# Kernel tuning notes

Measured on AMD Instinct MI355X. Metric: run time of the kernel, lower is better.

## Reference

```python
import jax, jax.numpy as jnp
import numpy as np

N_NODES = 100000
N_EDGES = 3200000
N_GRAPHS = 256
NEG_SLOPE = 0.2  # PyG GATConv default


def setup_inputs() -> dict:
    key = jax.random.key(0)
    ks = jax.random.split(key, 20)
    x = jax.random.normal(ks[0], (N_NODES, 20), jnp.float32)
    edge_index = jax.random.randint(ks[1], (2, N_EDGES), 0, N_NODES, dtype=jnp.int32)
    batch = jnp.sort(jax.random.randint(ks[2], (N_NODES,), 0, N_GRAPHS, dtype=jnp.int32))
    s = 0.1
    return {
        "x": x,
        "edge_index": edge_index,
        "batch": batch,
        "num_graphs": N_GRAPHS,
        "w_gat": jax.random.normal(ks[3], (20, 4, 16), jnp.float32) * s,
        "att_src": jax.random.normal(ks[4], (4, 16), jnp.float32) * s,
        "att_dst": jax.random.normal(ks[5], (4, 16), jnp.float32) * s,
        "b_gat": jax.random.normal(ks[6], (64,), jnp.float32) * s,
        "w_fuse": jax.random.normal(ks[7], (64, 64), jnp.float32) * s,
        "b_fuse": jax.random.normal(ks[8], (64,), jnp.float32) * s,
        "w_h1": jax.random.normal(ks[9], (64, 32), jnp.float32) * s,
        "b_h1": jax.random.normal(ks[10], (32,), jnp.float32) * s,
        "w_h2": jax.random.normal(ks[11], (32, 16), jnp.float32) * s,
        "b_h2": jax.random.normal(ks[12], (16,), jnp.float32) * s,
        "w_h3": jax.random.normal(ks[13], (16, 16), jnp.float32) * s,
        "b_h3": jax.random.normal(ks[14], (16,), jnp.float32) * s,
        "w_ev": jax.random.normal(ks[15], (16, 3), jnp.float32) * s,
        "b_ev": jax.random.normal(ks[16], (3,), jnp.float32) * s,
        "w_env": jax.random.normal(ks[17], (16, 3), jnp.float32) * s,
        "b_env": jax.random.normal(ks[18], (3,), jnp.float32) * s,
    }


def gat_conv(x, edge_index, w_gat, att_src, att_dst, b_gat, num_nodes):
    # Linear projection per head: [N, H, C]
    xh = jnp.einsum('nf,fhc->nhc', x, w_gat)
    # add self loops (PyG add_self_loops=True)
    loop = jnp.arange(num_nodes, dtype=edge_index.dtype)
    src = jnp.concatenate([edge_index[0], loop])  # source j
    dst = jnp.concatenate([edge_index[1], loop])  # target i
    # per-node attention terms [N, H]
    a_s = jnp.einsum('nhc,hc->nh', xh, att_src)
    a_d = jnp.einsum('nhc,hc->nh', xh, att_dst)
    # per-edge logit, leaky relu
    logit = jax.nn.leaky_relu(a_s[src] + a_d[dst], NEG_SLOPE)  # [E, H]
    # segment softmax over destination node
    m = jax.ops.segment_max(logit, dst, num_segments=num_nodes)
    e = jnp.exp(logit - m[dst])
    z = jax.ops.segment_sum(e, dst, num_segments=num_nodes)
    alpha = e / z[dst]  # [E, H]
    # weighted scatter-aggregate of source features
    msg = xh[src] * alpha[:, :, None]  # [E, H, C]
    out = jax.ops.segment_sum(msg, dst, num_segments=num_nodes)  # [N, H, C]
    return out.reshape(num_nodes, -1) + b_gat  # concat heads + bias


def reference(x, edge_index, batch, num_graphs, w_gat, att_src, att_dst, b_gat,
              w_fuse, b_fuse, w_h1, b_h1, w_h2, b_h2, w_h3, b_h3,
              w_ev, b_ev, w_env, b_env):
    n = x.shape[0]
    h = gat_conv(x, edge_index, w_gat, att_src, att_dst, b_gat, n)
    h = jax.nn.relu(h @ w_fuse + b_fuse)
    h = jax.nn.relu(h @ w_h1 + b_h1)
    h = jax.nn.relu(h @ w_h2 + b_h2)
    h = jax.nn.relu(h @ w_h3 + b_h3)
    # global mean pool over graphs
    sums = jax.ops.segment_sum(h, batch, num_segments=num_graphs)
    cnts = jax.ops.segment_sum(jnp.ones((n, 1), h.dtype), batch, num_segments=num_graphs)
    g = sums / jnp.maximum(cnts, 1.0)
    out_event = g @ w_ev + b_ev
    out_env = g @ w_env + b_env
    return (out_event, out_env)
```

## Files before the change

kernel.cpp:

```cpp
#include <hip/hip_runtime.h>
#include <hip/hip_bf16.h>
#include <hip/hip_fp16.h>

#define FIN 20
#define HEADS 4
#define F 64
#define NEG_SLOPE 0.2f
#define AP 68
#define BSHIFT 8
#define BMASK 255
#define BCAP 9216
#define MAXBUCK 512
#define BIN_EPT 16

__global__ void __launch_bounds__(256)
prep_bin(const float* __restrict__ x,
         const float* __restrict__ w_gat,
         const float* __restrict__ att_src,
         const float* __restrict__ att_dst,
         __half* __restrict__ xh,
         float* __restrict__ a_s,
         float* __restrict__ a_d,
         const int* __restrict__ ei, int E, int nbuck,
         int* __restrict__ gcount, int* __restrict__ bucketData,
         int n_nodes, int nbP)
{
    if (blockIdx.x < nbP) {
        __shared__ __align__(16) float w[FIN * F];
        __shared__ float asrc[F];
        __shared__ float adst[F];
        for (int i = threadIdx.x; i < FIN * F; i += 256) w[i] = w_gat[i];
        if (threadIdx.x < F) {
            asrc[threadIdx.x] = att_src[threadIdx.x];
            adst[threadIdx.x] = att_dst[threadIdx.x];
        }
        __syncthreads();

        int n = blockIdx.x * 256 + threadIdx.x;
        if (n >= n_nodes) return;

        float xv[FIN];
#pragma unroll
        for (int q = 0; q < FIN / 4; ++q) {
            float4 x4 = *(const float4*)&x[(size_t)n * FIN + q * 4];
            xv[q * 4 + 0] = x4.x; xv[q * 4 + 1] = x4.y;
            xv[q * 4 + 2] = x4.z; xv[q * 4 + 3] = x4.w;
        }

        float as[HEADS] = {0.f, 0.f, 0.f, 0.f};
        float ad[HEADS] = {0.f, 0.f, 0.f, 0.f};

#pragma unroll
        for (int j4 = 0; j4 < F / 4; ++j4) {
            float4 acc = make_float4(0.f, 0.f, 0.f, 0.f);
#pragma unroll
            for (int k = 0; k < FIN; ++k) {
                float4 w4 = *(const float4*)&w[k * F + j4 * 4];
                acc.x += xv[k] * w4.x;
                acc.y += xv[k] * w4.y;
                acc.z += xv[k] * w4.z;
                acc.w += xv[k] * w4.w;
            }
            __half2 p0 = __floats2half2_rn(acc.x, acc.y);
            __half2 p1 = __floats2half2_rn(acc.z, acc.w);
            float2 st;
            ((__half2*)&st)[0] = p0;
            ((__half2*)&st)[1] = p1;
            *(float2*)&xh[(size_t)n * F + j4 * 4] = st;

            int h = j4 >> 2;
            int jb = j4 * 4;
            as[h] += acc.x * asrc[jb] + acc.y * asrc[jb + 1] + acc.z * asrc[jb + 2] + acc.w * asrc[jb + 3];
            ad[h] += acc.x * adst[jb] + acc.y * adst[jb + 1] + acc.z * adst[jb + 2] + acc.w * adst[jb + 3];
        }
#pragma unroll
        for (int h = 0; h < HEADS; ++h) {
            a_s[(size_t)n * HEADS + h] = as[h];
            a_d[(size_t)n * HEADS + h] = ad[h];
        }
    } else {
        __shared__ int lcnt[MAXBUCK];
        __shared__ int lbase[MAXBUCK];
        for (int i = threadIdx.x; i < nbuck; i += 256) lcnt[i] = 0;
        __syncthreads();

        int base = (blockIdx.x - nbP) * (256 * BIN_EPT);
        int b_[BIN_EPT], w_[BIN_EPT];
#pragma unroll
        for (int j = 0; j < BIN_EPT; ++j) {
            int e = base + j * 256 + threadIdx.x;
            if (e < E) {
                int src = ei[e];
                int dst = ei[E + e];
                b_[j] = dst >> BSHIFT;
                w_[j] = ((dst & BMASK) << 17) | src;
                atomicAdd(&lcnt[b_[j]], 1);
            } else b_[j] = -1;
        }
        __syncthreads();
        for (int i = threadIdx.x; i < nbuck; i += 256) {
            int c = lcnt[i];
            lbase[i] = c ? atomicAdd(&gcount[i], c) : 0;
            lcnt[i] = 0;
        }
        __syncthreads();
#pragma unroll
        for (int j = 0; j < BIN_EPT; ++j) {
            if (b_[j] >= 0) {
                int p = lbase[b_[j]] + atomicAdd(&lcnt[b_[j]], 1);
                if (p < BCAP) bucketData[(size_t)b_[j] * BCAP + p] = w_[j];
            }
        }
    }
}

__global__ void __launch_bounds__(1024)
csr_build(const int* __restrict__ bucketData, const int* __restrict__ gcount,
          int* __restrict__ off, int* __restrict__ srcs,
          int n_nodes, int total_edges)
{
    __shared__ int hist[256];
    __shared__ int psum[256];
    int b = blockIdx.x;
    int t = threadIdx.x;
    int cnt = gcount[b]; if (cnt > BCAP) cnt = BCAP;
    int node0 = b << BSHIFT;
    int nnode = n_nodes - node0; if (nnode > 256) nnode = 256;

    if (t < 256) {
        int acc = 0;
        for (int i = t; i < b; i += 256) acc += gcount[i];
        psum[t] = acc;
    }
    __syncthreads();
    for (int d = 128; d > 0; d >>= 1) {
        if (t < d) psum[t] += psum[t + d];
        __syncthreads();
    }
    int base = psum[0] + node0;
    __syncthreads();
    if (b == 0 && t == 0) off[n_nodes] = total_edges;

    if (t < 256) hist[t] = 0;
    __syncthreads();
    const int* bd = bucketData + (size_t)b * BCAP;
    for (int i = t; i < cnt; i += 1024) atomicAdd(&hist[bd[i] >> 17], 1);
    __syncthreads();

    if (t < 256) psum[t] = (t < nnode) ? hist[t] + 1 : 0;
    __syncthreads();
    for (int d = 1; d < 256; d <<= 1) {
        int w = (t >= d && t < 256) ? psum[t - d] : 0;
        __syncthreads();
        if (t < 256) psum[t] += w;
        __syncthreads();
    }
    int ex = (t == 0 || t >= 256) ? 0 : psum[t - 1];
    __syncthreads();
    if (t < nnode) {
        int o = base + ex;
        off[node0 + t] = o;
        srcs[o] = node0 + t;
        hist[t] = o + 1;
    }
    __syncthreads();
    for (int i = t; i < cnt; i += 1024) {
        int w = bd[i];
        int p = atomicAdd(&hist[w >> 17], 1);
        srcs[p] = w & 0x1FFFF;
    }
}

__global__ void __launch_bounds__(256, 4)
gat_mlp(const int* __restrict__ off,
        const int* __restrict__ srcs,
        const float* __restrict__ a_s,
        const float* __restrict__ a_d,
        const __half* __restrict__ xh,
        const float* __restrict__ b_gat,
        const float* __restrict__ w_fuse, const float* __restrict__ b_fuse,
        const float* __restrict__ w_h1, const float* __restrict__ b_h1,
        const float* __restrict__ w_h2, const float* __restrict__ b_h2,
        const float* __restrict__ w_h3, const float* __restrict__ b_h3,
        float* __restrict__ rfeat,
        int n_nodes)
{
    __shared__ __align__(16) __half wfh[64 * 64];
    __shared__ __align__(16) __half w1h[64 * 32];
    __shared__ __align__(16) float w2[32 * 16];
    __shared__ __align__(16) float w3[16 * 16];
    __shared__ __align__(16) float bf[64];
    __shared__ __align__(16) float b1[32], b2[16], b3[16];
    __shared__ __align__(16) float act[32 * AP];

    for (int i = threadIdx.x; i < 64 * 64; i += 256) wfh[i] = __float2half(w_fuse[i]);
    for (int i = threadIdx.x; i < 64 * 32; i += 256) w1h[i] = __float2half(w_h1[i]);
    for (int i = threadIdx.x; i < 32 * 16; i += 256) w2[i] = w_h2[i];
    for (int i = threadIdx.x; i < 16 * 16; i += 256) w3[i] = w_h3[i];
    if (threadIdx.x < 64) bf[threadIdx.x] = b_fuse[threadIdx.x];
    else if (threadIdx.x < 96)  b1[threadIdx.x - 64] = b_h1[threadIdx.x - 64];
    else if (threadIdx.x < 112) b2[threadIdx.x - 96] = b_h2[threadIdx.x - 96];
    else if (threadIdx.x < 128) b3[threadIdx.x - 112] = b_h3[threadIdx.x - 112];

    {
        const int node_l2 = threadIdx.x >> 3;
        const int part = threadIdx.x & 7;
        const int n = blockIdx.x * 32 + node_l2;
        const int h = part >> 1;
        const int g8 = (threadIdx.x & 63) >> 3;

        float acc[8] = {0.f, 0.f, 0.f, 0.f, 0.f, 0.f, 0.f, 0.f};
        float zacc = 0.f;
        bool active = (n < n_nodes);
        if (active) {
            int kb = off[n];
            int ke = off[n + 1];
            float adh = a_d[n * 4 + h];

            int i0 = kb + part;          i0 = i0 < ke - 1 ? i0 : ke - 1;
            int sA = srcs[i0];
            int i1 = kb + 8 + part;      i1 = i1 < ke - 1 ? i1 : ke - 1;
            int sNxt = srcs[i1];

            int sj[8];
#pragma unroll
            for (int j = 0; j < 8; ++j) sj[j] = __shfl(sA, g8 * 8 + j, 64);
            float4 rawA[8]; float aslA[8];
#pragma unroll
            for (int j = 0; j < 8; ++j) {
                rawA[j] = *(const float4*)&xh[(size_t)sj[j] * F + part * 8];
                aslA[j] = a_s[sj[j] * 4 + h];
            }

            float4 rawB[8]; float aslB[8];
            int base = kb;
            while (true) {
                bool hasB = (base + 8 < ke);
                if (hasB) {
#pragma unroll
                    for (int j = 0; j < 8; ++j) sj[j] = __shfl(sNxt, g8 * 8 + j, 64);
#pragma unroll
                    for (int j = 0; j < 8; ++j) {
                        rawB[j] = *(const float4*)&xh[(size_t)sj[j] * F + part * 8];
                        aslB[j] = a_s[sj[j] * 4 + h];
                    }
                    int i2 = base + 16 + part;  i2 = i2 < ke - 1 ? i2 : ke - 1;
                    sNxt = srcs[i2];
                }
#pragma unroll
                for (int j = 0; j < 8; ++j) {
                    float l = aslA[j] + adh;
                    l = l > 0.f ? l : NEG_SLOPE * l;
                    float e = (base + j < ke) ? __expf(l) : 0.f;
                    zacc += e;
                    const __half2* hp = (const __half2*)&rawA[j];
                    float2 c0 = __half22float2(hp[0]);
                    float2 c1 = __half22float2(hp[1]);
                    float2 c2 = __half22float2(hp[2]);
                    float2 c3 = __half22float2(hp[3]);
                    acc[0] += e * c0.x; acc[1] += e * c0.y;
                    acc[2] += e * c1.x; acc[3] += e * c1.y;
                    acc[4] += e * c2.x; acc[5] += e * c2.y;
                    acc[6] += e * c3.x; acc[7] += e * c3.y;
                }
                base += 8;
                if (!hasB) break;

                bool hasC = (base + 8 < ke);
                if (hasC) {
#pragma unroll
                    for (int j = 0; j < 8; ++j) sj[j] = __shfl(sNxt, g8 * 8 + j, 64);
#pragma unroll
                    for (int j = 0; j < 8; ++j) {
                        rawA[j] = *(const float4*)&xh[(size_t)sj[j] * F + part * 8];
                        aslA[j] = a_s[sj[j] * 4 + h];
                    }
                    int i2 = base + 16 + part;  i2 = i2 < ke - 1 ? i2 : ke - 1;
                    sNxt = srcs[i2];
                }
#pragma unroll
                for (int j = 0; j < 8; ++j) {
                    float l = aslB[j] + adh;
                    l = l > 0.f ? l : NEG_SLOPE * l;
                    float e = (base + j < ke) ? __expf(l) : 0.f;
                    zacc += e;
                    const __half2* hp = (const __half2*)&rawB[j];
                    float2 c0 = __half22float2(hp[0]);
                    float2 c1 = __half22float2(hp[1]);
                    float2 c2 = __half22float2(hp[2]);
                    float2 c3 = __half22float2(hp[3]);
                    acc[0] += e * c0.x; acc[1] += e * c0.y;
                    acc[2] += e * c1.x; acc[3] += e * c1.y;
                    acc[4] += e * c2.x; acc[5] += e * c2.y;
                    acc[6] += e * c3.x; acc[7] += e * c3.y;
                }
                base += 8;
                if (!hasC) break;
            }
        }
        float inv = active ? (1.f / zacc) : 0.f;
        float4 bg0 = *(const float4*)&b_gat[part * 8];
        float4 bg1 = *(const float4*)&b_gat[part * 8 + 4];
        float4 o0, o1;
        o0.x = acc[0] * inv + bg0.x; o0.y = acc[1] * inv + bg0.y;
        o0.z = acc[2] * inv + bg0.z; o0.w = acc[3] * inv + bg0.w;
        o1.x = acc[4] * inv + bg1.x; o1.y = acc[5] * inv + bg1.y;
        o1.z = acc[6] * inv + bg1.z; o1.w = acc[7] * inv + bg1.w;
        *(float4*)&act[node_l2 * AP + part * 8]     = o0;
        *(float4*)&act[node_l2 * AP + part * 8 + 4] = o1;
    }
    __syncthreads();

    const int node_l = threadIdx.x >> 4;
    const int part   = threadIdx.x & 15;
    const int nA     = blockIdx.x * 32 + node_l;
    const int nB     = nA + 16;
    const bool actvA = (nA < n_nodes);
    const bool actvB = (nB < n_nodes);

    float* rowA = &act[node_l * AP];
    float* rowB = &act[(node_l + 16) * AP];

    {
        float4 aA = *(const float4*)&bf[part * 4];
        float4 aB = aA;
#pragma unroll
        for (int k4 = 0; k4 < 16; ++k4) {
            float4 hA = *(const float4*)&rowA[k4 * 4];
            float4 hB = *(const float4*)&rowB[k4 * 4];
#pragma unroll
            for (int q = 0; q < 4; ++q) {
                const __half2* wp = (const __half2*)&wfh[(k4 * 4 + q) * 64 + part * 4];
                float2 wlo = __half22float2(wp[0]);
                float2 whi = __half22float2(wp[1]);
                float hva = (q == 0) ? hA.x : (q == 1) ? hA.y : (q == 2) ? hA.z : hA.w;
                float hvb = (q == 0) ? hB.x : (q == 1) ? hB.y : (q == 2) ? hB.z : hB.w;
                aA.x += hva * wlo.x; aA.y += hva * wlo.y;
                aA.z += hva * whi.x; aA.w += hva * whi.y;
                aB.x += hvb * wlo.x; aB.y += hvb * wlo.y;
                aB.z += hvb * whi.x; aB.w += hvb * whi.y;
            }
        }
        aA.x = aA.x > 0.f ? aA.x : 0.f; aA.y = aA.y > 0.f ? aA.y : 0.f;
        aA.z = aA.z > 0.f ? aA.z : 0.f; aA.w = aA.w > 0.f ? aA.w : 0.f;
        aB.x = aB.x > 0.f ? aB.x : 0.f; aB.y = aB.y > 0.f ? aB.y : 0.f;
        aB.z = aB.z > 0.f ? aB.z : 0.f; aB.w = aB.w > 0.f ? aB.w : 0.f;
        *(float4*)&rowA[part * 4] = aA;
        *(float4*)&rowB[part * 4] = aB;
    }

    {
        float axA = b1[part * 2], ayA = b1[part * 2 + 1];
        float axB = axA, ayB = ayA;
#pragma unroll
        for (int k4 = 0; k4 < 16; ++k4) {
            float4 hA = *(const float4*)&rowA[k4 * 4];
            float4 hB = *(const float4*)&rowB[k4 * 4];
#pragma unroll
            for (int q = 0; q < 4; ++q) {
                float2 w2f = __half22float2(*(const __half2*)&w1h[(k4 * 4 + q) * 32 + part * 2]);
                float hva = (q == 0) ? hA.x : (q == 1) ? hA.y : (q == 2) ? hA.z : hA.w;
                float hvb = (q == 0) ? hB.x : (q == 1) ? hB.y : (q == 2) ? hB.z : hB.w;
                axA += hva * w2f.x; ayA += hva * w2f.y;
                axB += hvb * w2f.x; ayB += hvb * w2f.y;
            }
        }
        axA = axA > 0.f ? axA : 0.f; ayA = ayA > 0.f ? ayA : 0.f;
        axB = axB > 0.f ? axB : 0.f; ayB = ayB > 0.f ? ayB : 0.f;
        float2 uA; uA.x = axA; uA.y = ayA;
        float2 uB; uB.x = axB; uB.y = ayB;
        *(float2*)&rowA[part * 2] = uA;
        *(float2*)&rowB[part * 2] = uB;
    }

    {
        float aA = b2[part], aB = aA;
#pragma unroll
        for (int k4 = 0; k4 < 8; ++k4) {
            float4 hA = *(const float4*)&rowA[k4 * 4];
            float4 hB = *(const float4*)&rowB[k4 * 4];
            float w0 = w2[(k4 * 4 + 0) * 16 + part];
            float wq1 = w2[(k4 * 4 + 1) * 16 + part];
            float wq2 = w2[(k4 * 4 + 2) * 16 + part];
            float wq3 = w2[(k4 * 4 + 3) * 16 + part];
            aA += hA.x * w0 + hA.y * wq1 + hA.z * wq2 + hA.w * wq3;
            aB += hB.x * w0 + hB.y * wq1 + hB.z * wq2 + hB.w * wq3;
        }
        aA = aA > 0.f ? aA : 0.f;
        aB = aB > 0.f ? aB : 0.f;
        rowA[part] = aA;
        rowB[part] = aB;
    }

    float rA, rB;
    {
        float aA = b3[part], aB = aA;
#pragma unroll
        for (int k4 = 0; k4 < 4; ++k4) {
            float4 hA = *(const float4*)&rowA[k4 * 4];
            float4 hB = *(const float4*)&rowB[k4 * 4];
            float w0 = w3[(k4 * 4 + 0) * 16 + part];
            float wq1 = w3[(k4 * 4 + 1) * 16 + part];
            float wq2 = w3[(k4 * 4 + 2) * 16 + part];
            float wq3 = w3[(k4 * 4 + 3) * 16 + part];
            aA += hA.x * w0 + hA.y * wq1 + hA.z * wq2 + hA.w * wq3;
            aB += hB.x * w0 + hB.y * wq1 + hB.z * wq2 + hB.w * wq3;
        }
        rA = aA > 0.f ? aA : 0.f;
        rB = aB > 0.f ? aB : 0.f;
    }

    if (actvA) rfeat[(size_t)nA * 16 + part] = rA;
    if (actvB) rfeat[(size_t)nB * 16 + part] = rB;
}

__global__ void __launch_bounds__(256)
pool_head(const float* __restrict__ rfeat, const int* __restrict__ batch,
          const float* __restrict__ w_ev, const float* __restrict__ b_ev,
          const float* __restrict__ w_env, const float* __restrict__ b_env,
          float* __restrict__ out, int n_nodes, int n_graphs)
{
    __shared__ int s_bounds[2];
    __shared__ float partial[16][17];
    __shared__ float gvec[16];

    int g = blockIdx.x;
    if (threadIdx.x < 2) {
        int target = g + threadIdx.x;
        int lo = 0, hi = n_nodes;
        while (lo < hi) { int m = (lo + hi) >> 1; if (batch[m] < target) lo = m + 1; else hi = m; }
        s_bounds[threadIdx.x] = lo;
    }
    __syncthreads();
    int start = s_bounds[0], end = s_bounds[1];

    const int c = threadIdx.x & 15;
    const int w = threadIdx.x >> 4;
    float acc = 0.f;
    for (int i = start + w; i < end; i += 16)
        acc += rfeat[(size_t)i * 16 + c];
    partial[w][c] = acc;
    __syncthreads();

    if (threadIdx.x < 16) {
        float s = 0.f;
#pragma unroll
        for (int ww = 0; ww < 16; ++ww) s += partial[ww][threadIdx.x];
        float cnt = (float)(end - start);
        cnt = cnt > 1.f ? cnt : 1.f;
        gvec[threadIdx.x] = s / cnt;
    }
    __syncthreads();

    if (threadIdx.x < 3) {
        int j = threadIdx.x;
        float a = b_ev[j];
#pragma unroll
        for (int k = 0; k < 16; ++k) a += gvec[k] * w_ev[k * 3 + j];
        out[(size_t)g * 3 + j] = a;
    } else if (threadIdx.x < 6) {
        int j = threadIdx.x - 3;
        float a = b_env[j];
#pragma unroll
        for (int k = 0; k < 16; ++k) a += gvec[k] * w_env[k * 3 + j];
        out[(size_t)n_graphs * 3 + (size_t)g * 3 + j] = a;
    }
}

extern "C" void kernel_launch(void* const* d_in, const int* in_sizes, int n_in,
                              void* d_out, int out_size, void* d_ws, size_t ws_size,
                              hipStream_t stream)
{
    const float* x       = (const float*)d_in[0];
    const int*   ei      = (const int*)d_in[1];
    const int*   batch   = (const int*)d_in[2];
    const float* w_gat   = (const float*)d_in[4];
    const float* att_src = (const float*)d_in[5];
    const float* att_dst = (const float*)d_in[6];
    const float* b_gat   = (const float*)d_in[7];
    const float* w_fuse  = (const float*)d_in[8];
    const float* b_fuse  = (const float*)d_in[9];
    const float* w_h1    = (const float*)d_in[10];
    const float* b_h1    = (const float*)d_in[11];
    const float* w_h2    = (const float*)d_in[12];
    const float* b_h2    = (const float*)d_in[13];
    const float* w_h3    = (const float*)d_in[14];
    const float* b_h3    = (const float*)d_in[15];
    const float* w_ev    = (const float*)d_in[16];
    const float* b_ev    = (const float*)d_in[17];
    const float* w_env   = (const float*)d_in[18];
    const float* b_env   = (const float*)d_in[19];

    const int n_nodes  = in_sizes[0] / FIN;
    const int E        = in_sizes[1] / 2;
    const int n_graphs = 256;
    const int total    = E + n_nodes;
    const int nbuck    = (n_nodes + BMASK) >> BSHIFT;

    float* ws     = (float*)d_ws;
    __half* xh    = (__half*)ws;
    float* a_s    = ws   + (size_t)n_nodes * 32;
    float* a_d    = a_s  + (size_t)n_nodes * HEADS;
    float* rfeat  = a_d  + (size_t)n_nodes * HEADS;
    int*   off    = (int*)(rfeat + (size_t)n_nodes * 16);
    int*   srcs   = off    + n_nodes + 1;
    int*   gcount = srcs   + total;
    int*   bucketData = gcount + nbuck;

    hipMemsetAsync(gcount, 0, (size_t)nbuck * sizeof(int), stream);

    const int nbP = (n_nodes + 255) / 256;
    const int nbB = (E + 256 * BIN_EPT - 1) / (256 * BIN_EPT);

    prep_bin<<<nbP + nbB, 256, 0, stream>>>(
        x, w_gat, att_src, att_dst, xh, a_s, a_d,
        ei, E, nbuck, gcount, bucketData, n_nodes, nbP);

    csr_build<<<nbuck, 1024, 0, stream>>>(
        bucketData, gcount, off, srcs, n_nodes, total);

    gat_mlp<<<(n_nodes + 31) / 32, 256, 0, stream>>>(
        off, srcs, a_s, a_d, xh, b_gat,
        w_fuse, b_fuse, w_h1, b_h1, w_h2, b_h2, w_h3, b_h3,
        rfeat, n_nodes);

    pool_head<<<n_graphs, 256, 0, stream>>>(
        rfeat, batch, w_ev, b_ev, w_env, b_env, (float*)d_out, n_nodes, n_graphs);
}
```

Before: 269.4 us.

## Sort nodes by degree within buckets to balance GAT aggregation wavefronts

New measurement: 287.0 us. 6.5% more time.

```diff
diff --git a/kernel.cpp b/kernel.cpp
--- a/kernel.cpp
+++ b/kernel.cpp
@@ -117,10 +117,12 @@
 __global__ void __launch_bounds__(1024)
 csr_build(const int* __restrict__ bucketData, const int* __restrict__ gcount,
           int* __restrict__ off, int* __restrict__ srcs,
+          int* __restrict__ order,
           int n_nodes, int total_edges)
 {
     __shared__ int hist[256];
     __shared__ int psum[256];
+    __shared__ int skey[256];
     int b = blockIdx.x;
     int t = threadIdx.x;
     int cnt = gcount[b]; if (cnt > BCAP) cnt = BCAP;
@@ -147,7 +149,9 @@
     for (int i = t; i < cnt; i += 1024) atomicAdd(&hist[bd[i] >> 17], 1);
     __syncthreads();
 
-    if (t < 256) psum[t] = (t < nnode) ? hist[t] + 1 : 0;
+    int v = 0;
+    if (t < nnode) v = hist[t] + 1;
+    if (t < 256) psum[t] = v;
     __syncthreads();
     for (int d = 1; d < 256; d <<= 1) {
         int w = (t >= d && t < 256) ? psum[t - d] : 0;
@@ -169,11 +173,30 @@
         int p = atomicAdd(&hist[w >> 17], 1);
         srcs[p] = w & 0x1FFFF;
     }
+
+    __syncthreads();
+    if (t < 256) skey[t] = (t < nnode) ? ((v << 8) | t) : 0x7FFFFFFF;
+    __syncthreads();
+    for (int k = 2; k <= 256; k <<= 1) {
+        for (int j = k >> 1; j > 0; j >>= 1) {
+            if (t < 256) {
+                int ixj = t ^ j;
+                if (ixj > t) {
+                    int a0 = skey[t], a1 = skey[ixj];
+                    bool up = ((t & k) == 0);
+                    if (up ? (a0 > a1) : (a0 < a1)) { skey[t] = a1; skey[ixj] = a0; }
+                }
+            }
+            __syncthreads();
+        }
+    }
+    if (t < nnode) order[node0 + t] = node0 + (skey[t] & 0xFF);
 }
 
 __global__ void __launch_bounds__(256, 4)
 gat_mlp(const int* __restrict__ off,
         const int* __restrict__ srcs,
+        const int* __restrict__ order,
         const float* __restrict__ a_s,
         const float* __restrict__ a_d,
         const __half* __restrict__ xh,
@@ -205,14 +228,16 @@
     {
         const int node_l2 = threadIdx.x >> 3;
         const int part = threadIdx.x & 7;
-        const int n = blockIdx.x * 32 + node_l2;
+        const int oidx = blockIdx.x * 32 + node_l2;
         const int h = part >> 1;
         const int g8 = (threadIdx.x & 63) >> 3;
 
         float acc[8] = {0.f, 0.f, 0.f, 0.f, 0.f, 0.f, 0.f, 0.f};
         float zacc = 0.f;
-        bool active = (n < n_nodes);
+        bool active = (oidx < n_nodes);
+        int n = 0;
         if (active) {
+            n = order[oidx];
             int kb = off[n];
             int ke = off[n + 1];
             float adh = a_d[n * 4 + h];
@@ -313,10 +338,12 @@
 
     const int node_l = threadIdx.x >> 4;
     const int part   = threadIdx.x & 15;
-    const int nA     = blockIdx.x * 32 + node_l;
-    const int nB     = nA + 16;
-    const bool actvA = (nA < n_nodes);
-    const bool actvB = (nB < n_nodes);
+    const int oA     = blockIdx.x * 32 + node_l;
+    const int oB     = oA + 16;
+    const bool actvA = (oA < n_nodes);
+    const bool actvB = (oB < n_nodes);
+    const int nA     = actvA ? order[oA] : 0;
+    const int nB     = actvB ? order[oB] : 0;
 
     float* rowA = &act[node_l * AP];
     float* rowB = &act[(node_l + 16) * AP];
@@ -506,6 +533,7 @@
     int*   srcs   = off    + n_nodes + 1;
     int*   gcount = srcs   + total;
     int*   bucketData = gcount + nbuck;
+    int*   order  = bucketData + (size_t)nbuck * BCAP;
 
     hipMemsetAsync(gcount, 0, (size_t)nbuck * sizeof(int), stream);
 
@@ -517,10 +545,10 @@
         ei, E, nbuck, gcount, bucketData, n_nodes, nbP);
 
     csr_build<<<nbuck, 1024, 0, stream>>>(
-        bucketData, gcount, off, srcs, n_nodes, total);
+        bucketData, gcount, off, srcs, order, n_nodes, total);
 
     gat_mlp<<<(n_nodes + 31) / 32, 256, 0, stream>>>(
-        off, srcs, a_s, a_d, xh, b_gat,
+        off, srcs, order, a_s, a_d, xh, b_gat,
         w_fuse, b_fuse, w_h1, b_h1, w_h2, b_h2, w_h3, b_h3,
         rfeat, n_nodes);
 
```
